# Kernel optimization log

Hardware: AMD Instinct MI355X
Metric: run time of the kernel (lower is better)

## Reference

```python
import jax, jax.numpy as jnp
import numpy as np

N_NODES = 50000
N_EDGES = 800000
N_GRAPHS = 50
D_IN = 128
D_HID = 128
D_OUT = 10


def setup_inputs() -> dict:
    key = jax.random.key(0)
    ks = jax.random.split(key, 8)
    h = jax.random.normal(ks[0], (N_NODES, D_IN), dtype=jnp.float32)
    src = jax.random.randint(ks[1], (N_EDGES,), 0, N_NODES, dtype=jnp.int32)
    dst = jax.random.randint(ks[2], (N_EDGES,), 0, N_NODES, dtype=jnp.int32)
    graph_ids = jnp.sort(jax.random.randint(ks[3], (N_NODES,), 0, N_GRAPHS, dtype=jnp.int32))
    s = 1.0 / np.sqrt(D_HID)
    W1 = jax.random.normal(ks[4], (D_IN, D_HID), dtype=jnp.float32) * s
    W2 = jax.random.normal(ks[5], (D_HID, D_HID), dtype=jnp.float32) * s
    W3 = jax.random.normal(ks[6], (D_HID, D_HID), dtype=jnp.float32) * s
    Wm = jax.random.normal(ks[7], (D_HID, D_OUT), dtype=jnp.float32) * s
    return {
        "h": h, "src": src, "dst": dst, "graph_ids": graph_ids,
        "W1": W1, "b1": jnp.zeros((D_HID,), jnp.float32),
        "W2": W2, "b2": jnp.zeros((D_HID,), jnp.float32),
        "W3": W3, "b3": jnp.zeros((D_HID,), jnp.float32),
        "Wm": Wm, "bm": jnp.zeros((D_OUT,), jnp.float32),
    }


def _graph_conv(h, W, b, src, dst, norm_src, norm_dst):
    # DGL GraphConv, norm='both': out = D_dst^{-1/2} * A @ (D_src^{-1/2} * h) @ W + b
    m = (h * norm_src[:, None])[src]              # [E, d] gather (memory-bound)
    agg = jax.ops.segment_sum(m, dst, num_segments=N_NODES)  # [N, d] scatter-add
    return (agg * norm_dst[:, None]) @ W + b


def reference(h, src, dst, graph_ids, W1, b1, W2, b2, W3, b3, Wm, bm):
    ones_e = jnp.ones((N_EDGES,), jnp.float32)
    out_deg = jax.ops.segment_sum(ones_e, src, num_segments=N_NODES)
    in_deg = jax.ops.segment_sum(ones_e, dst, num_segments=N_NODES)
    norm_src = jnp.clip(out_deg, 1.0, None) ** -0.5
    norm_dst = jnp.clip(in_deg, 1.0, None) ** -0.5

    h = jax.nn.relu(_graph_conv(h, W1, b1, src, dst, norm_src, norm_dst))
    h = jax.nn.relu(_graph_conv(h, W2, b2, src, dst, norm_src, norm_dst))
    h = jax.nn.relu(_graph_conv(h, W3, b3, src, dst, norm_src, norm_dst))

    # mean-nodes readout per graph
    hg_sum = jax.ops.segment_sum(h, graph_ids, num_segments=N_GRAPHS)  # [G, d]
    cnt = jax.ops.segment_sum(jnp.ones((N_NODES,), jnp.float32), graph_ids, num_segments=N_GRAPHS)
    hg = hg_sum / jnp.clip(cnt, 1.0, None)[:, None]

    logits = hg @ Wm + bm                                 # [G, D_OUT]
    return jax.nn.log_softmax(logits, axis=0)             # faithful to dim=0 in source
```

## Files before the change

kernel.cpp:

```cpp
#include <hip/hip_runtime.h>

#define N_NODES 50000
#define N_EDGES 800000
#define N_GRAPHS 50
#define D 128
#define D_OUT 10
#define PLANE_F4 200000
#define NB 196
#define NBLK 196

__global__ __launch_bounds__(256) void part_hist_src(const int* __restrict__ src,
                                                     const int* __restrict__ dst,
                                                     int* __restrict__ gh,
                                                     int* __restrict__ out_deg) {
    __shared__ int lh[NB];
    int tid = threadIdx.x, blk = blockIdx.x;
    if (tid < NB) lh[tid] = 0;
    __syncthreads();
    int base = blk * 4096;
    #pragma unroll
    for (int j = 0; j < 16; j++) {
        int i = base + j * 256 + tid;
        if (i < N_EDGES) {
            atomicAdd(&out_deg[src[i]], 1);
            atomicAdd(&lh[dst[i] >> 8], 1);
        }
    }
    __syncthreads();
    if (tid < NB) gh[tid * NBLK + blk] = lh[tid];
}

__global__ __launch_bounds__(1024) void part_scan(int* __restrict__ gh) {
    __shared__ int wsum[16];
    __shared__ int carry_s;
    const int N = NB * NBLK;
    int tid = threadIdx.x;
    int lane = tid & 63, wid = tid >> 6;
    if (tid == 0) carry_s = 0;
    __syncthreads();
    for (int base = 0; base < N; base += 4096) {
        int i0 = base + tid * 4;
        int v0 = (i0 + 0 < N) ? gh[i0 + 0] : 0;
        int v1 = (i0 + 1 < N) ? gh[i0 + 1] : 0;
        int v2 = (i0 + 2 < N) ? gh[i0 + 2] : 0;
        int v3 = (i0 + 3 < N) ? gh[i0 + 3] : 0;
        int s = v0 + v1 + v2 + v3;
        int x = s;
        #pragma unroll
        for (int d = 1; d < 64; d <<= 1) {
            int y = __shfl_up(x, d, 64);
            if (lane >= d) x += y;
        }
        if (lane == 63) wsum[wid] = x;
        __syncthreads();
        if (wid == 0) {
            int t = (lane < 16) ? wsum[lane] : 0;
            #pragma unroll
            for (int d = 1; d < 16; d <<= 1) {
                int y = __shfl_up(t, d, 64);
                if (lane >= d) t += y;
            }
            if (lane < 16) wsum[lane] = t;
        }
        __syncthreads();
        int woff = (wid == 0) ? 0 : wsum[wid - 1];
        int run = carry_s + woff + (x - s);
        if (i0 + 0 < N) gh[i0 + 0] = run; run += v0;
        if (i0 + 1 < N) gh[i0 + 1] = run; run += v1;
        if (i0 + 2 < N) gh[i0 + 2] = run; run += v2;
        if (i0 + 3 < N) gh[i0 + 3] = run; run += v3;
        __syncthreads();
        if (tid == 0) carry_s += wsum[15];
        __syncthreads();
    }
}

__global__ __launch_bounds__(256) void part_scatter(const int* __restrict__ src,
                                                    const int* __restrict__ dst,
                                                    const int* __restrict__ gh,
                                                    unsigned int* __restrict__ packed) {
    __shared__ int lc[NB];
    int tid = threadIdx.x, blk = blockIdx.x;
    if (tid < NB) lc[tid] = gh[tid * NBLK + blk];
    __syncthreads();
    int base = blk * 4096;
    #pragma unroll
    for (int j = 0; j < 16; j++) {
        int i = base + j * 256 + tid;
        if (i < N_EDGES) {
            int d = dst[i];
            int s = src[i];
            int p = atomicAdd(&lc[d >> 8], 1);
            packed[p] = ((unsigned int)(d & 255) << 16) | (unsigned int)s;
        }
    }
}

__global__ __launch_bounds__(256) void bucket_csr(const unsigned int* __restrict__ packed,
                                                  const int* __restrict__ gh,
                                                  unsigned short* __restrict__ col16,
                                                  int* __restrict__ row_ptr,
                                                  float* __restrict__ nd) {
    __shared__ unsigned int ep[8192];
    __shared__ unsigned short lcol[8192];
    __shared__ int hist[256], cur[256], wsum[4];
    int t = threadIdx.x, b = blockIdx.x;
    int nb = gh[b * NBLK];
    int ne = (b < NB - 1) ? gh[(b + 1) * NBLK] : N_EDGES;
    int cnt = ne - nb;
    if (cnt > 8192) cnt = 8192;
    hist[t] = 0;
    __syncthreads();
    for (int i = t; i < cnt; i += 256) {
        unsigned int e = packed[nb + i];
        ep[i] = e;
        atomicAdd(&hist[e >> 16], 1);
    }
    __syncthreads();
    int v = hist[t];
    int lane = t & 63, w = t >> 6;
    int x = v;
    #pragma unroll
    for (int d = 1; d < 64; d <<= 1) {
        int y = __shfl_up(x, d, 64);
        if (lane >= d) x += y;
    }
    if (lane == 63) wsum[w] = x;
    __syncthreads();
    int add = 0;
    #pragma unroll
    for (int i = 0; i < 4; i++) if (i < w) add += wsum[i];
    int excl = add + x - v;
    cur[t] = excl;
    int node = b * 256 + t;
    if (node < N_NODES) {
        row_ptr[node] = nb + excl;
        int id = v > 1 ? v : 1;
        nd[node] = 1.0f / sqrtf((float)id);
    }
    if (b == NB - 1 && t == 0) row_ptr[N_NODES] = N_EDGES;
    __syncthreads();
    for (int i = t; i < cnt; i += 256) {
        unsigned int e = ep[i];
        int p = atomicAdd(&cur[e >> 16], 1);
        lcol[p] = (unsigned short)(e & 0xFFFF);
    }
    __syncthreads();
    for (int i = t; i < cnt; i += 256) col16[nb + i] = lcol[i];
}

__global__ __launch_bounds__(256) void prescale_k(const float* __restrict__ h,
                                                  const int* __restrict__ out_deg,
                                                  float* __restrict__ out) {
    int i = blockIdx.x * 256 + threadIdx.x;
    if (i < N_NODES * 32) {
        int node = i >> 5;
        int kg = i & 31;
        float4 v = ((const float4*)h)[i];
        int od = out_deg[node];
        float s = 1.0f / sqrtf((float)(od > 1 ? od : 1));
        int p = kg >> 2, q = kg & 3;
        ((float4*)out)[p * PLANE_F4 + node * 4 + q] =
            make_float4(v.x * s, v.y * s, v.z * s, v.w * s);
    }
}

__global__ __launch_bounds__(256) void spmm_k(const float* __restrict__ x,
                                              const int* __restrict__ row_ptr,
                                              const unsigned short* __restrict__ col,
                                              const float* __restrict__ nd,
                                              float* __restrict__ out) {
    int b = blockIdx.x;
    int slice = b & 7;
    int node = (b >> 3) * 64 + (threadIdx.x >> 2);
    if (node >= N_NODES) return;
    int q = threadIdx.x & 3;
    int s = row_ptr[node];
    int e = row_ptr[node + 1];
    const float4* xp = (const float4*)x + slice * PLANE_F4;
    float4 a0 = make_float4(0.f, 0.f, 0.f, 0.f);
    float4 a1 = make_float4(0.f, 0.f, 0.f, 0.f);
    int i = s;
    for (; i + 4 <= e; i += 4) {
        int c0 = col[i], c1 = col[i + 1], c2 = col[i + 2], c3 = col[i + 3];
        float4 h0 = xp[c0 * 4 + q];
        float4 h1 = xp[c1 * 4 + q];
        float4 h2 = xp[c2 * 4 + q];
        float4 h3 = xp[c3 * 4 + q];
        a0.x += h0.x; a0.y += h0.y; a0.z += h0.z; a0.w += h0.w;
        a1.x += h1.x; a1.y += h1.y; a1.z += h1.z; a1.w += h1.w;
        a0.x += h2.x; a0.y += h2.y; a0.z += h2.z; a0.w += h2.w;
        a1.x += h3.x; a1.y += h3.y; a1.z += h3.z; a1.w += h3.w;
    }
    for (; i < e; i++) {
        float4 hv = xp[col[i] * 4 + q];
        a0.x += hv.x; a0.y += hv.y; a0.z += hv.z; a0.w += hv.w;
    }
    float ndv = nd[node];
    ((float4*)out)[slice * PLANE_F4 + node * 4 + q] =
        make_float4((a0.x + a1.x) * ndv, (a0.y + a1.y) * ndv,
                    (a0.z + a1.z) * ndv, (a0.w + a1.w) * ndv);
}

template <int MODE>
__global__ __launch_bounds__(512) void gemm_relu_k(const float* __restrict__ A,
                                                   const float* __restrict__ W,
                                                   const float* __restrict__ bias,
                                                   const int* __restrict__ odeg,
                                                   float* __restrict__ out) {
    __shared__ float As_t[128 * 256];
    int tid = threadIdx.x;
    int row0 = blockIdx.x * 256;
    const float4* A4 = (const float4*)A;

    #pragma unroll
    for (int it = 0; it < 16; it++) {
        int linear = it * 512 + tid;
        int p = linear >> 10;
        int rem = linear & 1023;
        int r = rem >> 2;
        int q = rem & 3;
        int row = row0 + r;
        float4 a = (row < N_NODES) ? A4[p * PLANE_F4 + row * 4 + q]
                                   : make_float4(0.f, 0.f, 0.f, 0.f);
        int kb = p * 16 + q * 4;
        As_t[(kb + 0) * 256 + r] = a.x;
        As_t[(kb + 1) * 256 + r] = a.y;
        As_t[(kb + 2) * 256 + r] = a.z;
        As_t[(kb + 3) * 256 + r] = a.w;
    }
    __syncthreads();

    int tc = tid & 15;
    int tr = tid >> 4;
    float acc[8][8];
    #pragma unroll
    for (int r = 0; r < 8; r++)
        #pragma unroll
        for (int c = 0; c < 8; c++) acc[r][c] = 0.f;

    const float4* W4 = (const float4*)W;
    #pragma unroll 2
    for (int k = 0; k < 128; k++) {
        float4 w0 = W4[k * 32 + tc * 2];
        float4 w1 = W4[k * 32 + tc * 2 + 1];
        float4 a0 = *(const float4*)(As_t + k * 256 + tr * 8);
        float4 a1 = *(const float4*)(As_t + k * 256 + tr * 8 + 4);
        float av[8] = {a0.x, a0.y, a0.z, a0.w, a1.x, a1.y, a1.z, a1.w};
        float wv[8] = {w0.x, w0.y, w0.z, w0.w, w1.x, w1.y, w1.z, w1.w};
        #pragma unroll
        for (int rr = 0; rr < 8; rr++)
            #pragma unroll
            for (int cc = 0; cc < 8; cc++)
                acc[rr][cc] = fmaf(av[rr], wv[cc], acc[rr][cc]);
    }

    float4 bv0 = ((const float4*)bias)[tc * 2];
    float4 bv1 = ((const float4*)bias)[tc * 2 + 1];
    #pragma unroll
    for (int rr = 0; rr < 8; rr++) {
        int row = row0 + tr * 8 + rr;
        if (row < N_NODES) {
            float4 o0, o1;
            o0.x = fmaxf(acc[rr][0] + bv0.x, 0.f);
            o0.y = fmaxf(acc[rr][1] + bv0.y, 0.f);
            o0.z = fmaxf(acc[rr][2] + bv0.z, 0.f);
            o0.w = fmaxf(acc[rr][3] + bv0.w, 0.f);
            o1.x = fmaxf(acc[rr][4] + bv1.x, 0.f);
            o1.y = fmaxf(acc[rr][5] + bv1.y, 0.f);
            o1.z = fmaxf(acc[rr][6] + bv1.z, 0.f);
            o1.w = fmaxf(acc[rr][7] + bv1.w, 0.f);
            if (MODE == 0) {
                int od = odeg[row];
                float s = 1.0f / sqrtf((float)(od > 1 ? od : 1));
                o0.x *= s; o0.y *= s; o0.z *= s; o0.w *= s;
                o1.x *= s; o1.y *= s; o1.z *= s; o1.w *= s;
                int p = tc >> 1;
                int q0 = (tc & 1) * 2;
                ((float4*)out)[p * PLANE_F4 + row * 4 + q0] = o0;
                ((float4*)out)[p * PLANE_F4 + row * 4 + q0 + 1] = o1;
            } else {
                ((float4*)out)[row * 32 + tc * 2] = o0;
                ((float4*)out)[row * 32 + tc * 2 + 1] = o1;
            }
        }
    }
}

__global__ __launch_bounds__(256) void proj_readout_k(const float* __restrict__ h,
                                                      const int* __restrict__ gid,
                                                      const float* __restrict__ Wm,
                                                      float* __restrict__ hgp,
                                                      int* __restrict__ gcnt) {
    __shared__ float Wmt[10 * 144];
    int tid = threadIdx.x;
    for (int i = tid; i < 1280; i += 256) {
        int k = i / 10, o = i % 10;
        Wmt[o * 144 + k + 4 * (k >> 5)] = Wm[i];
    }
    __syncthreads();

    int v = blockIdx.x * 64 + (tid >> 2);
    int quarter = tid & 3;
    int lane = tid & 63;

    float acc[D_OUT];
    #pragma unroll
    for (int o = 0; o < D_OUT; o++) acc[o] = 0.f;
    int g = -1;
    int cnt = 0;
    if (v < N_NODES) {
        g = gid[v];
        cnt = (quarter == 0) ? 1 : 0;
        const float4* h4 = (const float4*)h + v * 32 + quarter * 8;
        const float* wbase = Wmt + quarter * 36;
        #pragma unroll
        for (int kk = 0; kk < 8; kk++) {
            float4 hv = h4[kk];
            #pragma unroll
            for (int o = 0; o < D_OUT; o++) {
                float4 w = *(const float4*)(wbase + o * 144 + kk * 4);
                acc[o] += hv.x * w.x + hv.y * w.y + hv.z * w.z + hv.w * w.w;
            }
        }
    }

    #pragma unroll
    for (int d = 1; d < 64; d <<= 1) {
        int gp = __shfl_up(g, d, 64);
        int cp = __shfl_up(cnt, d, 64);
        bool take = (lane >= d) && (gp == g);
        #pragma unroll
        for (int o = 0; o < D_OUT; o++) {
            float ap = __shfl_up(acc[o], d, 64);
            if (take) acc[o] += ap;
        }
        if (take) cnt += cp;
    }
    int gn = __shfl_down(g, 1, 64);
    bool tail = (lane == 63) || (gn != g);
    if (tail && g >= 0) {
        #pragma unroll
        for (int o = 0; o < D_OUT; o++) atomicAdd(&hgp[g * D_OUT + o], acc[o]);
        if (cnt > 0) atomicAdd(&gcnt[g], cnt);
    }
}

__global__ __launch_bounds__(512) void final_k(const float* __restrict__ hgp,
                                               const int* __restrict__ gcnt,
                                               const float* __restrict__ bm,
                                               float* __restrict__ out) {
    __shared__ float lg[N_GRAPHS * D_OUT];
    __shared__ float colm[D_OUT], colls[D_OUT];
    int tid = threadIdx.x;
    if (tid < N_GRAPHS * D_OUT) {
        int g = tid / D_OUT, o = tid % D_OUT;
        float c = (float)gcnt[g];
        lg[tid] = hgp[tid] / (c > 1.f ? c : 1.f) + bm[o];
    }
    __syncthreads();
    if (tid < D_OUT) {
        float m = -1e30f;
        for (int g = 0; g < N_GRAPHS; g++) m = fmaxf(m, lg[g * D_OUT + tid]);
        float s = 0.f;
        for (int g = 0; g < N_GRAPHS; g++) s += expf(lg[g * D_OUT + tid] - m);
        colm[tid] = m; colls[tid] = logf(s);
    }
    __syncthreads();
    if (tid < N_GRAPHS * D_OUT) {
        int o = tid % D_OUT;
        out[tid] = lg[tid] - colm[o] - colls[o];
    }
}

extern "C" void kernel_launch(void* const* d_in, const int* in_sizes, int n_in,
                              void* d_out, int out_size, void* d_ws, size_t ws_size,
                              hipStream_t stream) {
    const float* h_in = (const float*)d_in[0];
    const int*   src  = (const int*)d_in[1];
    const int*   dst  = (const int*)d_in[2];
    const int*   gid  = (const int*)d_in[3];
    const float* W1 = (const float*)d_in[4];  const float* b1 = (const float*)d_in[5];
    const float* W2 = (const float*)d_in[6];  const float* b2 = (const float*)d_in[7];
    const float* W3 = (const float*)d_in[8];  const float* b3 = (const float*)d_in[9];
    const float* Wm = (const float*)d_in[10]; const float* bm = (const float*)d_in[11];

    char* ws = (char*)d_ws;
    int*            row_ptr = (int*)(ws + 0);
    unsigned short* col16   = (unsigned short*)(ws + 200032);
    int*            out_deg = (int*)(ws + 1800032);
    float*          nd      = (float*)(ws + 2000032);
    int*            gcnt    = (int*)(ws + 2200032);
    float*          hgp     = (float*)(ws + 2200288);
    int*            gh      = (int*)(ws + 2202336);
    float*          bufA    = (float*)(ws + 2356000);
    float*          bufB    = (float*)(ws + 27956000);
    unsigned int*   packed  = (unsigned int*)bufB;

    hipMemsetAsync(out_deg, 0, 200000, stream);
    hipMemsetAsync(gcnt, 0, 2304, stream);

    part_hist_src<<<NBLK, 256, 0, stream>>>(src, dst, gh, out_deg);
    part_scan<<<1, 1024, 0, stream>>>(gh);
    part_scatter<<<NBLK, 256, 0, stream>>>(src, dst, gh, packed);
    bucket_csr<<<NB, 256, 0, stream>>>(packed, gh, col16, row_ptr, nd);
    prescale_k<<<6250, 256, 0, stream>>>(h_in, out_deg, bufA);

    spmm_k<<<6256, 256, 0, stream>>>(bufA, row_ptr, col16, nd, bufB);
    gemm_relu_k<0><<<196, 512, 0, stream>>>(bufB, W1, b1, out_deg, bufA);
    spmm_k<<<6256, 256, 0, stream>>>(bufA, row_ptr, col16, nd, bufB);
    gemm_relu_k<0><<<196, 512, 0, stream>>>(bufB, W2, b2, out_deg, bufA);
    spmm_k<<<6256, 256, 0, stream>>>(bufA, row_ptr, col16, nd, bufB);
    gemm_relu_k<1><<<196, 512, 0, stream>>>(bufB, W3, b3, out_deg, bufA);

    proj_readout_k<<<782, 256, 0, stream>>>(bufA, gid, Wm, hgp, gcnt);
    final_k<<<1, 512, 0, stream>>>(hgp, gcnt, bm, (float*)d_out);
}
```

Baseline: 474.4 us.

## Process four consecutive CSR rows per thread group in SpMM with merged edge stream

Each 4-lane group in the SpMM kernel now walks the combined edge range of four consecutive nodes, flushing the accumulator whenever a row boundary is crossed. The aim is to balance work across uneven row degrees and keep the 4-wide gather unroll busy across row boundaries, with a quarter as many blocks. The workspace layout is also reordered so out_deg and gcnt are adjacent, letting one memset replace two. The trade-offs are a branchy boundary loop inside the unrolled body and fewer independent accumulators.

```diff
diff --git a/kernel.cpp b/kernel.cpp
--- a/kernel.cpp
+++ b/kernel.cpp
@@ -172,34 +172,52 @@
                                               float* __restrict__ out) {
     int b = blockIdx.x;
     int slice = b & 7;
-    int node = (b >> 3) * 64 + (threadIdx.x >> 2);
-    if (node >= N_NODES) return;
+    int n0 = (b >> 3) * 256 + ((threadIdx.x >> 2) << 2);
+    if (n0 >= N_NODES) return;
     int q = threadIdx.x & 3;
-    int s = row_ptr[node];
-    int e = row_ptr[node + 1];
+    int nhi = n0 + 4; if (nhi > N_NODES) nhi = N_NODES;
+    int e    = row_ptr[n0];
+    int eend = row_ptr[nhi];
+    int cur  = n0;
+    int nbnd = row_ptr[cur + 1];
     const float4* xp = (const float4*)x + slice * PLANE_F4;
-    float4 a0 = make_float4(0.f, 0.f, 0.f, 0.f);
-    float4 a1 = make_float4(0.f, 0.f, 0.f, 0.f);
-    int i = s;
-    for (; i + 4 <= e; i += 4) {
-        int c0 = col[i], c1 = col[i + 1], c2 = col[i + 2], c3 = col[i + 3];
+    float4* op = (float4*)out + slice * PLANE_F4;
+    float4 acc = make_float4(0.f, 0.f, 0.f, 0.f);
+
+#define SPMM_STAGE(HV)                                                        \
+    while (e >= nbnd) {                                                       \
+        float nv = nd[cur];                                                   \
+        op[cur * 4 + q] = make_float4(acc.x * nv, acc.y * nv,                 \
+                                      acc.z * nv, acc.w * nv);                \
+        acc = make_float4(0.f, 0.f, 0.f, 0.f);                                \
+        ++cur; nbnd = row_ptr[cur + 1];                                       \
+    }                                                                         \
+    acc.x += HV.x; acc.y += HV.y; acc.z += HV.z; acc.w += HV.w;               \
+    ++e;
+
+    while (e + 4 <= eend) {
+        int c0 = col[e], c1 = col[e + 1], c2 = col[e + 2], c3 = col[e + 3];
         float4 h0 = xp[c0 * 4 + q];
         float4 h1 = xp[c1 * 4 + q];
         float4 h2 = xp[c2 * 4 + q];
         float4 h3 = xp[c3 * 4 + q];
-        a0.x += h0.x; a0.y += h0.y; a0.z += h0.z; a0.w += h0.w;
-        a1.x += h1.x; a1.y += h1.y; a1.z += h1.z; a1.w += h1.w;
-        a0.x += h2.x; a0.y += h2.y; a0.z += h2.z; a0.w += h2.w;
-        a1.x += h3.x; a1.y += h3.y; a1.z += h3.z; a1.w += h3.w;
-    }
-    for (; i < e; i++) {
-        float4 hv = xp[col[i] * 4 + q];
-        a0.x += hv.x; a0.y += hv.y; a0.z += hv.z; a0.w += hv.w;
-    }
-    float ndv = nd[node];
-    ((float4*)out)[slice * PLANE_F4 + node * 4 + q] =
-        make_float4((a0.x + a1.x) * ndv, (a0.y + a1.y) * ndv,
-                    (a0.z + a1.z) * ndv, (a0.w + a1.w) * ndv);
+        SPMM_STAGE(h0)
+        SPMM_STAGE(h1)
+        SPMM_STAGE(h2)
+        SPMM_STAGE(h3)
+    }
+    while (e < eend) {
+        int c0 = col[e];
+        float4 h0 = xp[c0 * 4 + q];
+        SPMM_STAGE(h0)
+    }
+#undef SPMM_STAGE
+    for (; cur < nhi; ++cur) {
+        float nv = nd[cur];
+        op[cur * 4 + q] = make_float4(acc.x * nv, acc.y * nv,
+                                      acc.z * nv, acc.w * nv);
+        acc = make_float4(0.f, 0.f, 0.f, 0.f);
+    }
 }
 
 template <int MODE>
@@ -388,8 +406,8 @@
     char* ws = (char*)d_ws;
     int*            row_ptr = (int*)(ws + 0);
     unsigned short* col16   = (unsigned short*)(ws + 200032);
-    int*            out_deg = (int*)(ws + 1800032);
-    float*          nd      = (float*)(ws + 2000032);
+    float*          nd      = (float*)(ws + 1800032);
+    int*            out_deg = (int*)(ws + 2000032);
     int*            gcnt    = (int*)(ws + 2200032);
     float*          hgp     = (float*)(ws + 2200288);
     int*            gh      = (int*)(ws + 2202336);
@@ -397,8 +415,7 @@
     float*          bufB    = (float*)(ws + 27956000);
     unsigned int*   packed  = (unsigned int*)bufB;
 
-    hipMemsetAsync(out_deg, 0, 200000, stream);
-    hipMemsetAsync(gcnt, 0, 2304, stream);
+    hipMemsetAsync(out_deg, 0, 202304, stream);
 
     part_hist_src<<<NBLK, 256, 0, stream>>>(src, dst, gh, out_deg);
     part_scan<<<1, 1024, 0, stream>>>(gh);
@@ -406,11 +423,11 @@
     bucket_csr<<<NB, 256, 0, stream>>>(packed, gh, col16, row_ptr, nd);
     prescale_k<<<6250, 256, 0, stream>>>(h_in, out_deg, bufA);
 
-    spmm_k<<<6256, 256, 0, stream>>>(bufA, row_ptr, col16, nd, bufB);
+    spmm_k<<<1568, 256, 0, stream>>>(bufA, row_ptr, col16, nd, bufB);
     gemm_relu_k<0><<<196, 512, 0, stream>>>(bufB, W1, b1, out_deg, bufA);
-    spmm_k<<<6256, 256, 0, stream>>>(bufA, row_ptr, col16, nd, bufB);
+    spmm_k<<<1568, 256, 0, stream>>>(bufA, row_ptr, col16, nd, bufB);
     gemm_relu_k<0><<<196, 512, 0, stream>>>(bufB, W2, b2, out_deg, bufA);
-    spmm_k<<<6256, 256, 0, stream>>>(bufA, row_ptr, col16, nd, bufB);
+    spmm_k<<<1568, 256, 0, stream>>>(bufA, row_ptr, col16, nd, bufB);
     gemm_relu_k<1><<<196, 512, 0, stream>>>(bufB, W3, b3, out_deg, bufA);
 
     proj_readout_k<<<782, 256, 0, stream>>>(bufA, gid, Wm, hgp, gcnt);
```

New measurement: 581.8 us. +22.6%, slower.
